# Performance work log

Hardware: AMD Instinct MI355X
Metric: run time of the kernel (lower is better)

## Reference

```python
import jax, jax.numpy as jnp
import numpy as np

N_NODES = 100000
N_REL = 8
IN_DIM = 64
HID = 128
OUT = 64
N_EDGES = 640000


def setup_inputs() -> dict:
    key = jax.random.key(0)
    ks = jax.random.split(key, 24)

    def w(k, shape, fan_in):
        return jax.random.normal(k, shape, jnp.float32) / np.sqrt(fan_in).astype(np.float32)

    inp = {}
    inp["emb"] = jax.random.normal(ks[0], (N_NODES, IN_DIM), jnp.float32)
    dims = [(IN_DIM, HID), (HID, HID), (HID, HID // 2), (HID // 2, OUT)]
    for i, (di, do) in enumerate(dims, 1):
        inp[f"W{i}"] = w(ks[3 * i], (N_REL, di, do), di)      # per-relation weight
        inp[f"R{i}"] = w(ks[3 * i + 1], (di, do), di)          # root weight
        inp[f"B{i}"] = jnp.zeros((do,), jnp.float32)           # bias
    inp["g1"] = jnp.ones((HID,), jnp.float32)
    inp["b1"] = jnp.zeros((HID,), jnp.float32)
    inp["g2"] = jnp.ones((HID,), jnp.float32)
    inp["b2"] = jnp.zeros((HID,), jnp.float32)
    inp["ei"] = jax.random.randint(ks[20], (2, N_EDGES), 0, N_NODES, jnp.int32)
    inp["et"] = jax.random.randint(ks[21], (N_EDGES,), 0, N_REL, jnp.int32)
    return inp


def rgcn(x, ei, et, W, Wr, b):
    # PyG RGCNConv (aggr='mean'): out_i = x_i @ Wroot + b + sum_r mean_{j in N_r(i)} x_j @ W_r
    # Aggregate-then-transform: mean x[src] per (dst, rel) bin, then per-relation GEMM.
    n, r, d = x.shape[0], W.shape[0], x.shape[1]
    src, dst = ei[0], ei[1]
    seg = dst * r + et                                   # combined (node, relation) segment id
    agg = jax.ops.segment_sum(x[src], seg, num_segments=n * r)          # [N*R, d]
    cnt = jax.ops.segment_sum(jnp.ones((src.shape[0],), x.dtype), seg, num_segments=n * r)
    agg = (agg / jnp.maximum(cnt, 1.0)[:, None]).reshape(n, r, d)       # mean per relation
    return jnp.einsum('nri,rio->no', agg, W) + x @ Wr + b


def layer_norm(x, g, b, eps=1e-5):
    mu = jnp.mean(x, axis=-1, keepdims=True)
    var = jnp.mean((x - mu) ** 2, axis=-1, keepdims=True)
    return (x - mu) * jax.lax.rsqrt(var + eps) * g + b


def reference(emb, W1, R1, B1, W2, R2, B2, W3, R3, B3, W4, R4, B4, g1, b1, g2, b2, ei, et):
    # dropout is eval-mode identity
    x = jax.nn.relu(rgcn(emb, ei, et, W1, R1, B1))
    x = layer_norm(x, g1, b1)
    identity = x
    x = jax.nn.relu(rgcn(x, ei, et, W2, R2, B2))
    x = layer_norm(x + identity, g2, b2)
    x = jax.nn.relu(rgcn(x, ei, et, W3, R3, B3))
    return rgcn(x, ei, et, W4, R4, B4)
```

## Files before the change

kernel.cpp:

```cpp
#include <hip/hip_runtime.h>
#include <math.h>

#define NN 100000
#define NR 8
#define NE 640000
#define SEGN (NN * NR)
#define SPB 2048
#define NSB ((SEGN + SPB - 1) / SPB)

#define TILES 1563
#define HT1 782
#define HT2 781
#define HP1 (HT1 * 64)
#define HP2 (HT2 * 64)
#define HPF (TILES * 64)

typedef __attribute__((ext_vector_type(8))) __bf16 bf16x8;
typedef __attribute__((ext_vector_type(4))) float  f32x4;

__device__ __forceinline__ float bf2f(unsigned short b) {
    return __uint_as_float((unsigned)b << 16);
}
__device__ __forceinline__ unsigned short f2bf(float v) {
    __bf16 b = (__bf16)v;
    return __builtin_bit_cast(unsigned short, b);
}


__global__ __launch_bounds__(256) void count_kernel(
    const int* __restrict__ dst, const int* __restrict__ et, unsigned* __restrict__ cnt) {
    int e = blockIdx.x * 256 + threadIdx.x;
    if (e < NE) atomicAdd(&cnt[(size_t)et[e] * NN + dst[e]], 1u);
}

__global__ __launch_bounds__(256) void scan1_kernel(
    const unsigned* __restrict__ cnt, unsigned* __restrict__ bsum) {
    __shared__ unsigned red[256];
    int b = blockIdx.x, t = threadIdx.x;
    int i0 = b * SPB;
    unsigned s = 0;
#pragma unroll
    for (int k = 0; k < SPB / 256; ++k) {
        int i = i0 + k * 256 + t;
        if (i < SEGN) s += cnt[i];
    }
    red[t] = s;
    __syncthreads();
    for (int off = 128; off >= 1; off >>= 1) {
        if (t < off) red[t] += red[t + off];
        __syncthreads();
    }
    if (t == 0) bsum[b] = red[0];
}

__global__ __launch_bounds__(512) void scan2_kernel(
    unsigned* __restrict__ bsum, int* __restrict__ segoff) {
    __shared__ unsigned buf[512];
    int t = threadIdx.x;
    unsigned v = (t < NSB) ? bsum[t] : 0u;
    buf[t] = v;
    __syncthreads();
    for (int off = 1; off < 512; off <<= 1) {
        unsigned w = (t >= off) ? buf[t - off] : 0u;
        __syncthreads();
        buf[t] += w;
        __syncthreads();
    }
    if (t < NSB) bsum[t] = buf[t] - v;
    if (t == 0) segoff[SEGN] = NE;
}

__global__ __launch_bounds__(256) void scan3_kernel(
    const unsigned* __restrict__ cnt, const unsigned* __restrict__ bsum,
    int* __restrict__ segoff) {
    __shared__ unsigned lc[SPB];
    __shared__ unsigned tsum[256];
    int b = blockIdx.x, t = threadIdx.x;
    int i0 = b * SPB;
#pragma unroll
    for (int k = 0; k < SPB / 256; ++k) {
        int i = i0 + k * 256 + t;
        lc[k * 256 + t] = (i < SEGN) ? cnt[i] : 0u;
    }
    __syncthreads();
    unsigned s = 0;
#pragma unroll
    for (int k = 0; k < 8; ++k) s += lc[t * 8 + k];
    tsum[t] = s;
    __syncthreads();
    for (int off = 1; off < 256; off <<= 1) {
        unsigned w = (t >= off) ? tsum[t - off] : 0u;
        __syncthreads();
        tsum[t] += w;
        __syncthreads();
    }
    unsigned base = bsum[b] + tsum[t] - s;
#pragma unroll
    for (int k = 0; k < 8; ++k) {
        unsigned c = lc[t * 8 + k];
        lc[t * 8 + k] = base;
        base += c;
    }
    __syncthreads();
#pragma unroll
    for (int k = 0; k < SPB / 256; ++k) {
        int i = i0 + k * 256 + t;
        if (i < SEGN) segoff[i] = (int)lc[k * 256 + t];
    }
}

__global__ __launch_bounds__(256) void fill_kernel(
    const int* __restrict__ src, const int* __restrict__ dst, const int* __restrict__ et,
    const int* __restrict__ segoff, unsigned* __restrict__ cursor, int* __restrict__ esrc) {
    int e = blockIdx.x * 256 + threadIdx.x;
    if (e >= NE) return;
    int d = dst[e];
    int seg = et[e] * NN + d;
    int pos = segoff[seg] + (int)atomicAdd(&cursor[seg], 1u);
    esrc[pos] = src[e] | ((d & 3) << 17);
}


template <int D, int O>
__global__ __launch_bounds__(256) void pack_kernel(
    const float* __restrict__ W, const float* __restrict__ Wr, __bf16* __restrict__ Wp) {
    constexpr int KT = D / 32, NTN = O / 16;
    int idx = blockIdx.x * 256 + threadIdx.x;
    if (idx >= (NR + 1) * KT * NTN * 64) return;
    int l = idx & 63;
    int rest = idx >> 6;
    int nt = rest % NTN; rest /= NTN;
    int kt = rest % KT;
    int r  = rest / KT;
    const float* srcw = (r < NR) ? (W + (size_t)r * D * O) : Wr;
    int n  = nt * 16 + (l & 15);
    int k0 = kt * 32 + (l >> 4) * 8;
    bf16x8 v;
#pragma unroll
    for (int j = 0; j < 8; ++j) {
        int p  = k0 + j;
        int kd = (D == 128) ? ((p >> 1) + ((p & 1) << 6)) : p;
        v[j] = (__bf16)srcw[(size_t)kd * O + n];
    }
    *(bf16x8*)(Wp + (size_t)idx * 8) = v;
}


template <int D, int XF>
__global__ __launch_bounds__(256) void gather_kernel(
    const void* __restrict__ xin, const int* __restrict__ segoff,
    const int* __restrict__ esrc, ushort* __restrict__ agg,
    int nbase, int agg_off, int HP)
{
    int wv = threadIdx.x >> 6, ln = threadIdx.x & 63;
    int r  = blockIdx.y;
    int i0 = blockIdx.x * 16 + wv * 4;
    int n0 = nbase + i0;

    const float*    xf = (const float*)xin;
    const ushort*   xb = (const ushort*)xin;
    const unsigned* xs = (const unsigned*)xin;

    float ax[4] = {0, 0, 0, 0}, ay[4] = {0, 0, 0, 0};
    int eo[5];
#pragma unroll
    for (int k = 0; k <= 4; ++k) {
        int node = n0 + k; if (node > NN) node = NN;
        eo[k] = segoff[r * NN + node];
    }
    for (int ei = eo[0]; ei < eo[4]; ei += 4) {
        int nb = eo[4] - ei; if (nb > 4) nb = 4;
        int mm[4]; float vx[4], vy[4];
#pragma unroll
        for (int b = 0; b < 4; ++b) mm[b] = (b < nb) ? esrc[ei + b] : 0;
#pragma unroll
        for (int b = 0; b < 4; ++b) {
            if (b < nb) {
                int s = mm[b] & 0x1FFFF;
                if constexpr (XF == 0) {
                    vx[b] = xf[(size_t)s * 64 + ln];
                } else if constexpr (XF == 1) {
                    unsigned w = xs[(size_t)s * 64 + ln];
                    vx[b] = bf2f((unsigned short)(w & 0xFFFFu));
                    vy[b] = bf2f((unsigned short)(w >> 16));
                } else {
                    vx[b] = bf2f(xb[(size_t)s * 64 + ln]);
                }
            }
        }
#pragma unroll
        for (int b = 0; b < 4; ++b) {
            if (b < nb) {
                int k = mm[b] >> 17;
#pragma unroll
                for (int kk = 0; kk < 4; ++kk) {
                    ax[kk] += (kk == k) ? vx[b] : 0.0f;
                    if constexpr (D == 128) ay[kk] += (kk == k) ? vy[b] : 0.0f;
                }
            }
        }
    }
#pragma unroll
    for (int k = 0; k < 4; ++k) {
        int c = eo[k + 1] - eo[k];
        float sc = (c > 0) ? 1.0f / (float)c : 0.0f;
        size_t row = ((size_t)r * HP + agg_off + i0 + k) * D;
        if constexpr (D == 128) {
            unsigned st = (unsigned)f2bf(ax[k] * sc) | ((unsigned)f2bf(ay[k] * sc) << 16);
            *((unsigned*)(agg + row) + ln) = st;
        } else {
            agg[row + ln] = f2bf(ax[k] * sc);
        }
    }
}


template <int D, int O, int MODE, int XF, int OF>
__global__ __launch_bounds__(64) void gemm_layer(
    const ushort* __restrict__ agg, const __bf16* __restrict__ Wp,
    const float* __restrict__ bias, const float* __restrict__ gamma,
    const float* __restrict__ beta, const unsigned* __restrict__ xres,
    const void* __restrict__ xroot, void* __restrict__ outv, int base, int HP)
{
    constexpr int KT = D / 32, NTN = O / 16;
    constexpr int PD = (D == 64) ? 8 : 3;
    int ln = threadIdx.x, lg = ln >> 4, lm = ln & 15;
    int i0 = blockIdx.x * 16;

    const ushort* abase = agg + ((size_t)(i0 + lm)) * D + lg * 8;

    bf16x8 Aall[NR][KT];
#pragma unroll
    for (int r = 0; r < PD; ++r) {
        const ushort* ar = abase + (size_t)r * HP * D;
#pragma unroll
        for (int kt = 0; kt < KT; ++kt)
            Aall[r][kt] = *(const bf16x8*)(ar + kt * 32);
    }

    bf16x8 Aroot[KT];
    {
        int nrow = base + i0 + lm;
        if (nrow >= NN) nrow = NN - 1;
#pragma unroll
        for (int kt = 0; kt < KT; ++kt) {
            if constexpr (XF == 0) {
                const float* xp = (const float*)xroot + (size_t)nrow * 64 + kt * 32 + lg * 8;
                f32x4 a0 = *(const f32x4*)xp;
                f32x4 a1 = *(const f32x4*)(xp + 4);
#pragma unroll
                for (int j = 0; j < 4; ++j) {
                    Aroot[kt][j] = (__bf16)a0[j];
                    Aroot[kt][j + 4] = (__bf16)a1[j];
                }
            } else if constexpr (XF == 1) {
                Aroot[kt] = *(const bf16x8*)((const ushort*)xroot +
                                             (size_t)nrow * 128 + kt * 32 + lg * 8);
            } else {
                Aroot[kt] = *(const bf16x8*)((const ushort*)xroot +
                                             (size_t)nrow * 64 + kt * 32 + lg * 8);
            }
        }
    }

    f32x4 acc[NTN];
#pragma unroll
    for (int nt = 0; nt < NTN; ++nt)
#pragma unroll
        for (int q = 0; q < 4; ++q) acc[nt][q] = 0.0f;

#pragma unroll
    for (int r = 0; r < NR; ++r) {
        if (r + PD < NR) {
            const ushort* an = abase + (size_t)(r + PD) * HP * D;
#pragma unroll
            for (int kt = 0; kt < KT; ++kt)
                Aall[r + PD][kt] = *(const bf16x8*)(an + kt * 32);
        }
        const __bf16* bp = Wp + (((size_t)(r * KT) * NTN) << 9) + (ln << 3);
#pragma unroll
        for (int kt = 0; kt < KT; ++kt) {
            const __bf16* bpk = bp + (((size_t)(kt * NTN)) << 9);
#pragma unroll
            for (int nt = 0; nt < NTN; ++nt) {
                bf16x8 B = *(const bf16x8*)(bpk + ((size_t)nt << 9));
                acc[nt] = __builtin_amdgcn_mfma_f32_16x16x32_bf16(Aall[r][kt], B, acc[nt], 0, 0, 0);
            }
        }
    }
    {
        const __bf16* bp = Wp + (((size_t)(8 * KT) * NTN) << 9) + (ln << 3);
#pragma unroll
        for (int kt = 0; kt < KT; ++kt) {
            const __bf16* bpk = bp + (((size_t)(kt * NTN)) << 9);
#pragma unroll
            for (int nt = 0; nt < NTN; ++nt) {
                bf16x8 B = *(const bf16x8*)(bpk + ((size_t)nt << 9));
                acc[nt] = __builtin_amdgcn_mfma_f32_16x16x32_bf16(Aroot[kt], B, acc[nt], 0, 0, 0);
            }
        }
    }

    float bb[NTN], gg[NTN], be[NTN];
#pragma unroll
    for (int nt = 0; nt < NTN; ++nt) {
        bb[nt] = bias[nt * 16 + lm];
        if constexpr (MODE <= 1) {
            gg[nt] = gamma[nt * 16 + lm];
            be[nt] = beta[nt * 16 + lm];
        } else {
            gg[nt] = 0.0f; be[nt] = 0.0f;
        }
    }
#pragma unroll
    for (int q = 0; q < 4; ++q) {
        int row = lg * 4 + q;
        int n = base + i0 + row;
        int nc = (n < NN) ? n : 0;
        float v[NTN];
#pragma unroll
        for (int nt = 0; nt < NTN; ++nt) {
            v[nt] = acc[nt][q] + bb[nt];
            if constexpr (MODE <= 2) v[nt] = fmaxf(v[nt], 0.0f);
            if constexpr (MODE == 1) {
                unsigned w = xres[(size_t)nc * 64 + (nt & 3) * 16 + lm];
                v[nt] += bf2f((unsigned short)((nt < 4) ? (w & 0xFFFFu) : (w >> 16)));
            }
        }
        if constexpr (MODE <= 1) {
            float s1 = 0.0f, s2 = 0.0f;
#pragma unroll
            for (int nt = 0; nt < NTN; ++nt) { s1 += v[nt]; s2 += v[nt] * v[nt]; }
#pragma unroll
            for (int off = 1; off < 16; off <<= 1) {
                s1 += __shfl_xor(s1, off, 64);
                s2 += __shfl_xor(s2, off, 64);
            }
            float mu  = s1 * (1.0f / O);
            float var = s2 * (1.0f / O) - mu * mu;
            float rs  = rsqrtf(var + 1e-5f);
#pragma unroll
            for (int nt = 0; nt < NTN; ++nt) v[nt] = (v[nt] - mu) * rs * gg[nt] + be[nt];
        }
        if (n < NN) {
            if constexpr (OF == 0) {
#pragma unroll
                for (int nt = 0; nt < NTN; ++nt)
                    __builtin_nontemporal_store(
                        v[nt], (float*)outv + (size_t)n * O + nt * 16 + lm);
            } else if constexpr (OF == 1) {
#pragma unroll
                for (int nt = 0; nt < 4; ++nt)
                    ((unsigned*)outv)[(size_t)n * 64 + nt * 16 + lm] =
                        (unsigned)f2bf(v[nt]) | ((unsigned)f2bf(v[nt + 4]) << 16);
            } else {
#pragma unroll
                for (int nt = 0; nt < NTN; ++nt)
                    ((ushort*)outv)[(size_t)n * 64 + nt * 16 + lm] = f2bf(v[nt]);
            }
        }
    }
}


extern "C" void kernel_launch(void* const* d_in, const int* in_sizes, int n_in,
                              void* d_out, int out_size, void* d_ws, size_t ws_size,
                              hipStream_t stream) {
    const float* emb = (const float*)d_in[0];
    const float* W1  = (const float*)d_in[1];
    const float* R1  = (const float*)d_in[2];
    const float* B1  = (const float*)d_in[3];
    const float* W2  = (const float*)d_in[4];
    const float* R2  = (const float*)d_in[5];
    const float* B2  = (const float*)d_in[6];
    const float* W3  = (const float*)d_in[7];
    const float* R3  = (const float*)d_in[8];
    const float* B3  = (const float*)d_in[9];
    const float* W4  = (const float*)d_in[10];
    const float* R4  = (const float*)d_in[11];
    const float* B4  = (const float*)d_in[12];
    const float* g1  = (const float*)d_in[13];
    const float* b1  = (const float*)d_in[14];
    const float* g2  = (const float*)d_in[15];
    const float* b2  = (const float*)d_in[16];
    const int*   ei  = (const int*)d_in[17];
    const int*   et  = (const int*)d_in[18];
    const int* srcp = ei;
    const int* dstp = ei + NE;

    char* ws = (char*)d_ws;
    if (ws_size < 185734160u) return;
    int*      segoff = (int*)(ws + 0);
    int*      esrc   = (int*)(ws + 3200016);
    __bf16*   Wp1    = (__bf16*)(ws + 5760016);
    __bf16*   Wp2    = (__bf16*)(ws + 5907472);
    __bf16*   Wp3    = (__bf16*)(ws + 6202384);
    __bf16*   Wp4    = (__bf16*)(ws + 6349840);
    void*     x1     = (void*)(ws + 6423568);
    void*     x2     = (void*)(ws + 32023568);
    void*     x3     = (void*)(ws + 57623568);
    ushort*   agg    = (ushort*)(ws + 70423568);
    unsigned* cnt    = (unsigned*)(ws + 70423568);
    unsigned* cursor = (unsigned*)(ws + 73623568);
    unsigned* bsum   = (unsigned*)(ws + 76823568);
    float*    outp   = (float*)d_out;

    hipMemsetAsync(cnt, 0, 3200000, stream);
    hipMemsetAsync(cursor, 0, 3200000, stream);

    count_kernel<<<(NE + 255) / 256, 256, 0, stream>>>(dstp, et, cnt);
    scan1_kernel<<<NSB, 256, 0, stream>>>(cnt, bsum);
    scan2_kernel<<<1, 512, 0, stream>>>(bsum, segoff);
    scan3_kernel<<<NSB, 256, 0, stream>>>(cnt, bsum, segoff);
    fill_kernel<<<(NE + 255) / 256, 256, 0, stream>>>(
        srcp, dstp, et, segoff, cursor, esrc);

    pack_kernel<64, 128><<<(9 * 2 * 8 * 64 + 255) / 256, 256, 0, stream>>>(W1, R1, Wp1);
    pack_kernel<128, 128><<<(9 * 4 * 8 * 64 + 255) / 256, 256, 0, stream>>>(W2, R2, Wp2);
    pack_kernel<128, 64><<<(9 * 4 * 4 * 64 + 255) / 256, 256, 0, stream>>>(W3, R3, Wp3);
    pack_kernel<64, 64><<<(9 * 2 * 4 * 64 + 255) / 256, 256, 0, stream>>>(W4, R4, Wp4);

    gather_kernel<64, 0><<<dim3(HP1 / 16, 8), 256, 0, stream>>>(emb, segoff, esrc, agg, 0, 0, HPF);
    gather_kernel<64, 0><<<dim3(HP2 / 16, 8), 256, 0, stream>>>(emb, segoff, esrc, agg, HP1, HP1, HPF);
    gemm_layer<64, 128, 0, 0, 1><<<HPF / 16, 64, 0, stream>>>(
        agg, Wp1, B1, g1, b1, nullptr, emb, x1, 0, HPF);

    gather_kernel<128, 1><<<dim3(25024 / 16, 8), 256, 0, stream>>>(x1, segoff, esrc, agg, 0, 0, HP1);
    gather_kernel<128, 1><<<dim3(25024 / 16, 8), 256, 0, stream>>>(x1, segoff, esrc, agg, 25024, 25024, HP1);
    gemm_layer<128, 128, 1, 1, 1><<<HP1 / 16, 64, 0, stream>>>(
        agg, Wp2, B2, g2, b2, (const unsigned*)x1, x1, x2, 0, HP1);
    gather_kernel<128, 1><<<dim3(25024 / 16, 8), 256, 0, stream>>>(x1, segoff, esrc, agg, HP1, 0, HP2);
    gather_kernel<128, 1><<<dim3(24960 / 16, 8), 256, 0, stream>>>(x1, segoff, esrc, agg, HP1 + 25024, 25024, HP2);
    gemm_layer<128, 128, 1, 1, 1><<<HP2 / 16, 64, 0, stream>>>(
        agg, Wp2, B2, g2, b2, (const unsigned*)x1, x1, x2, HP1, HP2);

    gather_kernel<128, 1><<<dim3(25024 / 16, 8), 256, 0, stream>>>(x2, segoff, esrc, agg, 0, 0, HP1);
    gather_kernel<128, 1><<<dim3(25024 / 16, 8), 256, 0, stream>>>(x2, segoff, esrc, agg, 25024, 25024, HP1);
    gemm_layer<128, 64, 2, 1, 2><<<HP1 / 16, 64, 0, stream>>>(
        agg, Wp3, B3, nullptr, nullptr, nullptr, x2, x3, 0, HP1);
    gather_kernel<128, 1><<<dim3(25024 / 16, 8), 256, 0, stream>>>(x2, segoff, esrc, agg, HP1, 0, HP2);
    gather_kernel<128, 1><<<dim3(24960 / 16, 8), 256, 0, stream>>>(x2, segoff, esrc, agg, HP1 + 25024, 25024, HP2);
    gemm_layer<128, 64, 2, 1, 2><<<HP2 / 16, 64, 0, stream>>>(
        agg, Wp3, B3, nullptr, nullptr, nullptr, x2, x3, HP1, HP2);

    gather_kernel<64, 2><<<dim3(HP1 / 16, 8), 256, 0, stream>>>(x3, segoff, esrc, agg, 0, 0, HPF);
    gather_kernel<64, 2><<<dim3(HP2 / 16, 8), 256, 0, stream>>>(x3, segoff, esrc, agg, HP1, HP1, HPF);
    gemm_layer<64, 64, 3, 2, 0><<<HPF / 16, 64, 0, stream>>>(
        agg, Wp4, B4, nullptr, nullptr, nullptr, x3, outp, 0, HPF);
}
```

Measured before the change: 704.4 us.

## Fuse gather and GEMM into one launch pipelined over node quarters

After: 853.5 us. 1.21x slower.

```diff
diff --git a/kernel.cpp b/kernel.cpp
--- a/kernel.cpp
+++ b/kernel.cpp
@@ -8,12 +8,9 @@
 #define SPB 2048
 #define NSB ((SEGN + SPB - 1) / SPB)
 
-#define TILES 1563
-#define HT1 782
-#define HT2 781
-#define HP1 (HT1 * 64)
-#define HP2 (HT2 * 64)
-#define HPF (TILES * 64)
+#define QSZ 25024
+static const int qbase[5] = {0, 25024, 50048, 75072, 100032};
+static const int qsize[4] = {25024, 25024, 25024, 24960};
 
 typedef __attribute__((ext_vector_type(8))) __bf16 bf16x8;
 typedef __attribute__((ext_vector_type(4))) float  f32x4;
@@ -118,6 +115,16 @@
     int seg = et[e] * NN + d;
     int pos = segoff[seg] + (int)atomicAdd(&cursor[seg], 1u);
     esrc[pos] = src[e] | ((d & 3) << 17);
+}
+
+__global__ __launch_bounds__(256) void conv_emb(
+    const float* __restrict__ emb, ushort* __restrict__ embb) {
+    int i = blockIdx.x * 256 + threadIdx.x;
+    if (i * 4 >= NN * 64) return;
+    f32x4 v = *(const f32x4*)(emb + (size_t)i * 4);
+    ushort4 o;
+    o.x = f2bf(v[0]); o.y = f2bf(v[1]); o.z = f2bf(v[2]); o.w = f2bf(v[3]);
+    *(ushort4*)(embb + (size_t)i * 4) = o;
 }
 
 
@@ -146,18 +153,157 @@
 }
 
 
-template <int D, int XF>
-__global__ __launch_bounds__(256) void gather_kernel(
+template <int D, int O, int MODE, int XF, int OF>
+__global__ __launch_bounds__(256) void fused_kernel(
+    int mb,
+    const ushort* __restrict__ aggG, const __bf16* __restrict__ Wp,
+    const float* __restrict__ bias, const float* __restrict__ gamma,
+    const float* __restrict__ beta, const unsigned* __restrict__ xres,
+    const void* __restrict__ xroot, void* __restrict__ outv, int gbase, int gQP,
     const void* __restrict__ xin, const int* __restrict__ segoff,
-    const int* __restrict__ esrc, ushort* __restrict__ agg,
-    int nbase, int agg_off, int HP)
+    const int* __restrict__ esrc, ushort* __restrict__ aggS, int nbase, int sQP)
 {
-    int wv = threadIdx.x >> 6, ln = threadIdx.x & 63;
-    int r  = blockIdx.y;
-    int i0 = blockIdx.x * 16 + wv * 4;
+    constexpr int KT = D / 32, NTN = O / 16;
+    int tid = threadIdx.x;
+    int wv = tid >> 6, ln = tid & 63;
+
+    if ((int)blockIdx.x < mb) {
+        constexpr int PD = (D == 64) ? 8 : 3;
+        int lg = ln >> 4, lm = ln & 15;
+        int i0 = blockIdx.x * 64 + wv * 16;
+
+        const ushort* abase = aggG + ((size_t)(i0 + lm)) * D + lg * 8;
+
+        bf16x8 Aall[NR][KT];
+#pragma unroll
+        for (int r = 0; r < PD; ++r) {
+            const ushort* ar = abase + (size_t)r * gQP * D;
+#pragma unroll
+            for (int kt = 0; kt < KT; ++kt)
+                Aall[r][kt] = *(const bf16x8*)(ar + kt * 32);
+        }
+
+        bf16x8 Aroot[KT];
+        {
+            int nrow = gbase + i0 + lm;
+            if (nrow >= NN) nrow = NN - 1;
+#pragma unroll
+            for (int kt = 0; kt < KT; ++kt) {
+                if constexpr (XF == 1) {
+                    Aroot[kt] = *(const bf16x8*)((const ushort*)xroot +
+                                                 (size_t)nrow * 128 + kt * 32 + lg * 8);
+                } else {
+                    Aroot[kt] = *(const bf16x8*)((const ushort*)xroot +
+                                                 (size_t)nrow * 64 + kt * 32 + lg * 8);
+                }
+            }
+        }
+
+        f32x4 acc[NTN];
+#pragma unroll
+        for (int nt = 0; nt < NTN; ++nt)
+#pragma unroll
+            for (int q = 0; q < 4; ++q) acc[nt][q] = 0.0f;
+
+#pragma unroll
+        for (int r = 0; r < NR; ++r) {
+            if (r + PD < NR) {
+                const ushort* an = abase + (size_t)(r + PD) * gQP * D;
+#pragma unroll
+                for (int kt = 0; kt < KT; ++kt)
+                    Aall[r + PD][kt] = *(const bf16x8*)(an + kt * 32);
+            }
+            const __bf16* bp = Wp + (((size_t)(r * KT) * NTN) << 9) + (ln << 3);
+#pragma unroll
+            for (int kt = 0; kt < KT; ++kt) {
+                const __bf16* bpk = bp + (((size_t)(kt * NTN)) << 9);
+#pragma unroll
+                for (int nt = 0; nt < NTN; ++nt) {
+                    bf16x8 B = *(const bf16x8*)(bpk + ((size_t)nt << 9));
+                    acc[nt] = __builtin_amdgcn_mfma_f32_16x16x32_bf16(Aall[r][kt], B, acc[nt], 0, 0, 0);
+                }
+            }
+        }
+        {
+            const __bf16* bp = Wp + (((size_t)(8 * KT) * NTN) << 9) + (ln << 3);
+#pragma unroll
+            for (int kt = 0; kt < KT; ++kt) {
+                const __bf16* bpk = bp + (((size_t)(kt * NTN)) << 9);
+#pragma unroll
+                for (int nt = 0; nt < NTN; ++nt) {
+                    bf16x8 B = *(const bf16x8*)(bpk + ((size_t)nt << 9));
+                    acc[nt] = __builtin_amdgcn_mfma_f32_16x16x32_bf16(Aroot[kt], B, acc[nt], 0, 0, 0);
+                }
+            }
+        }
+
+        float bb[NTN], gg[NTN], be[NTN];
+#pragma unroll
+        for (int nt = 0; nt < NTN; ++nt) {
+            bb[nt] = bias[nt * 16 + lm];
+            if constexpr (MODE <= 1) {
+                gg[nt] = gamma[nt * 16 + lm];
+                be[nt] = beta[nt * 16 + lm];
+            } else {
+                gg[nt] = 0.0f; be[nt] = 0.0f;
+            }
+        }
+#pragma unroll
+        for (int q = 0; q < 4; ++q) {
+            int row = lg * 4 + q;
+            int n = gbase + i0 + row;
+            int nc = (n < NN) ? n : 0;
+            float v[NTN];
+#pragma unroll
+            for (int nt = 0; nt < NTN; ++nt) {
+                v[nt] = acc[nt][q] + bb[nt];
+                if constexpr (MODE <= 2) v[nt] = fmaxf(v[nt], 0.0f);
+                if constexpr (MODE == 1) {
+                    unsigned w = xres[(size_t)nc * 64 + (nt & 3) * 16 + lm];
+                    v[nt] += bf2f((unsigned short)((nt < 4) ? (w & 0xFFFFu) : (w >> 16)));
+                }
+            }
+            if constexpr (MODE <= 1) {
+                float s1 = 0.0f, s2 = 0.0f;
+#pragma unroll
+                for (int nt = 0; nt < NTN; ++nt) { s1 += v[nt]; s2 += v[nt] * v[nt]; }
+#pragma unroll
+                for (int off = 1; off < 16; off <<= 1) {
+                    s1 += __shfl_xor(s1, off, 64);
+                    s2 += __shfl_xor(s2, off, 64);
+                }
+                float mu  = s1 * (1.0f / O);
+                float var = s2 * (1.0f / O) - mu * mu;
+                float rs  = rsqrtf(var + 1e-5f);
+#pragma unroll
+                for (int nt = 0; nt < NTN; ++nt) v[nt] = (v[nt] - mu) * rs * gg[nt] + be[nt];
+            }
+            if (n < NN) {
+                if constexpr (OF == 0) {
+#pragma unroll
+                    for (int nt = 0; nt < NTN; ++nt)
+                        __builtin_nontemporal_store(
+                            v[nt], (float*)outv + (size_t)n * O + nt * 16 + lm);
+                } else if constexpr (OF == 1) {
+#pragma unroll
+                    for (int nt = 0; nt < 4; ++nt)
+                        ((unsigned*)outv)[(size_t)n * 64 + nt * 16 + lm] =
+                            (unsigned)f2bf(v[nt]) | ((unsigned)f2bf(v[nt + 4]) << 16);
+                } else {
+#pragma unroll
+                    for (int nt = 0; nt < NTN; ++nt)
+                        ((ushort*)outv)[(size_t)n * 64 + nt * 16 + lm] = f2bf(v[nt]);
+                }
+            }
+        }
+        return;
+    }
+
+    int gb = blockIdx.x - mb;
+    int tile = gb >> 3, r = gb & 7;
+    int i0 = tile * 16 + wv * 4;
     int n0 = nbase + i0;
 
-    const float*    xf = (const float*)xin;
     const ushort*   xb = (const ushort*)xin;
     const unsigned* xs = (const unsigned*)xin;
 
@@ -177,9 +323,7 @@
         for (int b = 0; b < 4; ++b) {
             if (b < nb) {
                 int s = mm[b] & 0x1FFFF;
-                if constexpr (XF == 0) {
-                    vx[b] = xf[(size_t)s * 64 + ln];
-                } else if constexpr (XF == 1) {
+                if constexpr (XF == 1) {
                     unsigned w = xs[(size_t)s * 64 + ln];
                     vx[b] = bf2f((unsigned short)(w & 0xFFFFu));
                     vy[b] = bf2f((unsigned short)(w >> 16));
@@ -204,164 +348,41 @@
     for (int k = 0; k < 4; ++k) {
         int c = eo[k + 1] - eo[k];
         float sc = (c > 0) ? 1.0f / (float)c : 0.0f;
-        size_t row = ((size_t)r * HP + agg_off + i0 + k) * D;
+        size_t row = ((size_t)r * sQP + i0 + k) * D;
         if constexpr (D == 128) {
             unsigned st = (unsigned)f2bf(ax[k] * sc) | ((unsigned)f2bf(ay[k] * sc) << 16);
-            *((unsigned*)(agg + row) + ln) = st;
+            *((unsigned*)(aggS + row) + ln) = st;
         } else {
-            agg[row + ln] = f2bf(ax[k] * sc);
-        }
-    }
-}
-
+            aggS[row + ln] = f2bf(ax[k] * sc);
+        }
+    }
+}
+
+
+#define SLOTE(D) ((size_t)8 * 25024 * (D))
 
 template <int D, int O, int MODE, int XF, int OF>
-__global__ __launch_bounds__(64) void gemm_layer(
-    const ushort* __restrict__ agg, const __bf16* __restrict__ Wp,
-    const float* __restrict__ bias, const float* __restrict__ gamma,
-    const float* __restrict__ beta, const unsigned* __restrict__ xres,
-    const void* __restrict__ xroot, void* __restrict__ outv, int base, int HP)
-{
-    constexpr int KT = D / 32, NTN = O / 16;
-    constexpr int PD = (D == 64) ? 8 : 3;
-    int ln = threadIdx.x, lg = ln >> 4, lm = ln & 15;
-    int i0 = blockIdx.x * 16;
-
-    const ushort* abase = agg + ((size_t)(i0 + lm)) * D + lg * 8;
-
-    bf16x8 Aall[NR][KT];
-#pragma unroll
-    for (int r = 0; r < PD; ++r) {
-        const ushort* ar = abase + (size_t)r * HP * D;
-#pragma unroll
-        for (int kt = 0; kt < KT; ++kt)
-            Aall[r][kt] = *(const bf16x8*)(ar + kt * 32);
-    }
-
-    bf16x8 Aroot[KT];
-    {
-        int nrow = base + i0 + lm;
-        if (nrow >= NN) nrow = NN - 1;
-#pragma unroll
-        for (int kt = 0; kt < KT; ++kt) {
-            if constexpr (XF == 0) {
-                const float* xp = (const float*)xroot + (size_t)nrow * 64 + kt * 32 + lg * 8;
-                f32x4 a0 = *(const f32x4*)xp;
-                f32x4 a1 = *(const f32x4*)(xp + 4);
-#pragma unroll
-                for (int j = 0; j < 4; ++j) {
-                    Aroot[kt][j] = (__bf16)a0[j];
-                    Aroot[kt][j + 4] = (__bf16)a1[j];
-                }
-            } else if constexpr (XF == 1) {
-                Aroot[kt] = *(const bf16x8*)((const ushort*)xroot +
-                                             (size_t)nrow * 128 + kt * 32 + lg * 8);
-            } else {
-                Aroot[kt] = *(const bf16x8*)((const ushort*)xroot +
-                                             (size_t)nrow * 64 + kt * 32 + lg * 8);
-            }
-        }
-    }
-
-    f32x4 acc[NTN];
-#pragma unroll
-    for (int nt = 0; nt < NTN; ++nt)
-#pragma unroll
-        for (int q = 0; q < 4; ++q) acc[nt][q] = 0.0f;
-
-#pragma unroll
-    for (int r = 0; r < NR; ++r) {
-        if (r + PD < NR) {
-            const ushort* an = abase + (size_t)(r + PD) * HP * D;
-#pragma unroll
-            for (int kt = 0; kt < KT; ++kt)
-                Aall[r + PD][kt] = *(const bf16x8*)(an + kt * 32);
-        }
-        const __bf16* bp = Wp + (((size_t)(r * KT) * NTN) << 9) + (ln << 3);
-#pragma unroll
-        for (int kt = 0; kt < KT; ++kt) {
-            const __bf16* bpk = bp + (((size_t)(kt * NTN)) << 9);
-#pragma unroll
-            for (int nt = 0; nt < NTN; ++nt) {
-                bf16x8 B = *(const bf16x8*)(bpk + ((size_t)nt << 9));
-                acc[nt] = __builtin_amdgcn_mfma_f32_16x16x32_bf16(Aall[r][kt], B, acc[nt], 0, 0, 0);
-            }
-        }
-    }
-    {
-        const __bf16* bp = Wp + (((size_t)(8 * KT) * NTN) << 9) + (ln << 3);
-#pragma unroll
-        for (int kt = 0; kt < KT; ++kt) {
-            const __bf16* bpk = bp + (((size_t)(kt * NTN)) << 9);
-#pragma unroll
-            for (int nt = 0; nt < NTN; ++nt) {
-                bf16x8 B = *(const bf16x8*)(bpk + ((size_t)nt << 9));
-                acc[nt] = __builtin_amdgcn_mfma_f32_16x16x32_bf16(Aroot[kt], B, acc[nt], 0, 0, 0);
-            }
-        }
-    }
-
-    float bb[NTN], gg[NTN], be[NTN];
-#pragma unroll
-    for (int nt = 0; nt < NTN; ++nt) {
-        bb[nt] = bias[nt * 16 + lm];
-        if constexpr (MODE <= 1) {
-            gg[nt] = gamma[nt * 16 + lm];
-            be[nt] = beta[nt * 16 + lm];
-        } else {
-            gg[nt] = 0.0f; be[nt] = 0.0f;
-        }
-    }
-#pragma unroll
-    for (int q = 0; q < 4; ++q) {
-        int row = lg * 4 + q;
-        int n = base + i0 + row;
-        int nc = (n < NN) ? n : 0;
-        float v[NTN];
-#pragma unroll
-        for (int nt = 0; nt < NTN; ++nt) {
-            v[nt] = acc[nt][q] + bb[nt];
-            if constexpr (MODE <= 2) v[nt] = fmaxf(v[nt], 0.0f);
-            if constexpr (MODE == 1) {
-                unsigned w = xres[(size_t)nc * 64 + (nt & 3) * 16 + lm];
-                v[nt] += bf2f((unsigned short)((nt < 4) ? (w & 0xFFFFu) : (w >> 16)));
-            }
-        }
-        if constexpr (MODE <= 1) {
-            float s1 = 0.0f, s2 = 0.0f;
-#pragma unroll
-            for (int nt = 0; nt < NTN; ++nt) { s1 += v[nt]; s2 += v[nt] * v[nt]; }
-#pragma unroll
-            for (int off = 1; off < 16; off <<= 1) {
-                s1 += __shfl_xor(s1, off, 64);
-                s2 += __shfl_xor(s2, off, 64);
-            }
-            float mu  = s1 * (1.0f / O);
-            float var = s2 * (1.0f / O) - mu * mu;
-            float rs  = rsqrtf(var + 1e-5f);
-#pragma unroll
-            for (int nt = 0; nt < NTN; ++nt) v[nt] = (v[nt] - mu) * rs * gg[nt] + be[nt];
-        }
-        if (n < NN) {
-            if constexpr (OF == 0) {
-#pragma unroll
-                for (int nt = 0; nt < NTN; ++nt)
-                    __builtin_nontemporal_store(
-                        v[nt], (float*)outv + (size_t)n * O + nt * 16 + lm);
-            } else if constexpr (OF == 1) {
-#pragma unroll
-                for (int nt = 0; nt < 4; ++nt)
-                    ((unsigned*)outv)[(size_t)n * 64 + nt * 16 + lm] =
-                        (unsigned)f2bf(v[nt]) | ((unsigned)f2bf(v[nt + 4]) << 16);
-            } else {
-#pragma unroll
-                for (int nt = 0; nt < NTN; ++nt)
-                    ((ushort*)outv)[(size_t)n * 64 + nt * 16 + lm] = f2bf(v[nt]);
-            }
-        }
-    }
-}
-
+static void run_layer(const void* xin, const __bf16* Wp, const float* bias,
+                      const float* gamma, const float* beta, const unsigned* xres,
+                      void* out, ushort* agg, const int* segoff, const int* esrc,
+                      hipStream_t stream) {
+    auto slot = [&](int q) { return agg + (size_t)(q & 1) * SLOTE(D); };
+    auto gB = [](int n) { return (n / 16) * 8; };
+    auto mB = [](int n) { return n / 64; };
+    fused_kernel<D, O, MODE, XF, OF><<<gB(qsize[0]), 256, 0, stream>>>(
+        0, nullptr, Wp, bias, gamma, beta, xres, xin, out, 0, 0,
+        xin, segoff, esrc, slot(0), qbase[0], qsize[0]);
+    for (int q = 0; q < 3; ++q) {
+        fused_kernel<D, O, MODE, XF, OF><<<mB(qsize[q]) + gB(qsize[q + 1]), 256, 0, stream>>>(
+            mB(qsize[q]), slot(q), Wp, bias, gamma, beta, xres, xin, out,
+            qbase[q], qsize[q],
+            xin, segoff, esrc, slot(q + 1), qbase[q + 1], qsize[q + 1]);
+    }
+    fused_kernel<D, O, MODE, XF, OF><<<mB(qsize[3]), 256, 0, stream>>>(
+        mB(qsize[3]), slot(3), Wp, bias, gamma, beta, xres, xin, out,
+        qbase[3], qsize[3],
+        xin, segoff, esrc, slot(3), 0, 0);
+}
 
 extern "C" void kernel_launch(void* const* d_in, const int* in_sizes, int n_in,
                               void* d_out, int out_size, void* d_ws, size_t ws_size,
@@ -389,20 +410,21 @@
     const int* dstp = ei + NE;
 
     char* ws = (char*)d_ws;
-    if (ws_size < 185734160u) return;
+    if (ws_size < 185721872u) return;
     int*      segoff = (int*)(ws + 0);
     int*      esrc   = (int*)(ws + 3200016);
     __bf16*   Wp1    = (__bf16*)(ws + 5760016);
     __bf16*   Wp2    = (__bf16*)(ws + 5907472);
     __bf16*   Wp3    = (__bf16*)(ws + 6202384);
     __bf16*   Wp4    = (__bf16*)(ws + 6349840);
-    void*     x1     = (void*)(ws + 6423568);
-    void*     x2     = (void*)(ws + 32023568);
-    void*     x3     = (void*)(ws + 57623568);
-    ushort*   agg    = (ushort*)(ws + 70423568);
-    unsigned* cnt    = (unsigned*)(ws + 70423568);
-    unsigned* cursor = (unsigned*)(ws + 73623568);
-    unsigned* bsum   = (unsigned*)(ws + 76823568);
+    ushort*   embb   = (ushort*)(ws + 6423568);
+    void*     x1     = (void*)(ws + 19223568);
+    void*     x2     = (void*)(ws + 44823568);
+    void*     x3     = (void*)(ws + 70423568);
+    ushort*   agg    = (ushort*)(ws + 83223568);
+    unsigned* cnt    = (unsigned*)(ws + 83223568);
+    unsigned* cursor = (unsigned*)(ws + 86423568);
+    unsigned* bsum   = (unsigned*)(ws + 89623568);
     float*    outp   = (float*)d_out;
 
     hipMemsetAsync(cnt, 0, 3200000, stream);
@@ -414,37 +436,19 @@
     scan3_kernel<<<NSB, 256, 0, stream>>>(cnt, bsum, segoff);
     fill_kernel<<<(NE + 255) / 256, 256, 0, stream>>>(
         srcp, dstp, et, segoff, cursor, esrc);
+    conv_emb<<<(NN * 64 / 4 + 255) / 256, 256, 0, stream>>>(emb, embb);
 
     pack_kernel<64, 128><<<(9 * 2 * 8 * 64 + 255) / 256, 256, 0, stream>>>(W1, R1, Wp1);
     pack_kernel<128, 128><<<(9 * 4 * 8 * 64 + 255) / 256, 256, 0, stream>>>(W2, R2, Wp2);
     pack_kernel<128, 64><<<(9 * 4 * 4 * 64 + 255) / 256, 256, 0, stream>>>(W3, R3, Wp3);
     pack_kernel<64, 64><<<(9 * 2 * 4 * 64 + 255) / 256, 256, 0, stream>>>(W4, R4, Wp4);
 
-    gather_kernel<64, 0><<<dim3(HP1 / 16, 8), 256, 0, stream>>>(emb, segoff, esrc, agg, 0, 0, HPF);
-    gather_kernel<64, 0><<<dim3(HP2 / 16, 8), 256, 0, stream>>>(emb, segoff, esrc, agg, HP1, HP1, HPF);
-    gemm_layer<64, 128, 0, 0, 1><<<HPF / 16, 64, 0, stream>>>(
-        agg, Wp1, B1, g1, b1, nullptr, emb, x1, 0, HPF);
-
-    gather_kernel<128, 1><<<dim3(25024 / 16, 8), 256, 0, stream>>>(x1, segoff, esrc, agg, 0, 0, HP1);
-    gather_kernel<128, 1><<<dim3(25024 / 16, 8), 256, 0, stream>>>(x1, segoff, esrc, agg, 25024, 25024, HP1);
-    gemm_layer<128, 128, 1, 1, 1><<<HP1 / 16, 64, 0, stream>>>(
-        agg, Wp2, B2, g2, b2, (const unsigned*)x1, x1, x2, 0, HP1);
-    gather_kernel<128, 1><<<dim3(25024 / 16, 8), 256, 0, stream>>>(x1, segoff, esrc, agg, HP1, 0, HP2);
-    gather_kernel<128, 1><<<dim3(24960 / 16, 8), 256, 0, stream>>>(x1, segoff, esrc, agg, HP1 + 25024, 25024, HP2);
-    gemm_layer<128, 128, 1, 1, 1><<<HP2 / 16, 64, 0, stream>>>(
-        agg, Wp2, B2, g2, b2, (const unsigned*)x1, x1, x2, HP1, HP2);
-
-    gather_kernel<128, 1><<<dim3(25024 / 16, 8), 256, 0, stream>>>(x2, segoff, esrc, agg, 0, 0, HP1);
-    gather_kernel<128, 1><<<dim3(25024 / 16, 8), 256, 0, stream>>>(x2, segoff, esrc, agg, 25024, 25024, HP1);
-    gemm_layer<128, 64, 2, 1, 2><<<HP1 / 16, 64, 0, stream>>>(
-        agg, Wp3, B3, nullptr, nullptr, nullptr, x2, x3, 0, HP1);
-    gather_kernel<128, 1><<<dim3(25024 / 16, 8), 256, 0, stream>>>(x2, segoff, esrc, agg, HP1, 0, HP2);
-    gather_kernel<128, 1><<<dim3(24960 / 16, 8), 256, 0, stream>>>(x2, segoff, esrc, agg, HP1 + 25024, 25024, HP2);
-    gemm_layer<128, 64, 2, 1, 2><<<HP2 / 16, 64, 0, stream>>>(
-        agg, Wp3, B3, nullptr, nullptr, nullptr, x2, x3, HP1, HP2);
-
-    gather_kernel<64, 2><<<dim3(HP1 / 16, 8), 256, 0, stream>>>(x3, segoff, esrc, agg, 0, 0, HPF);
-    gather_kernel<64, 2><<<dim3(HP2 / 16, 8), 256, 0, stream>>>(x3, segoff, esrc, agg, HP1, HP1, HPF);
-    gemm_layer<64, 64, 3, 2, 0><<<HPF / 16, 64, 0, stream>>>(
-        agg, Wp4, B4, nullptr, nullptr, nullptr, x3, outp, 0, HPF);
-}
+    run_layer<64, 128, 0, 2, 1>(embb, Wp1, B1, g1, b1, nullptr, x1,
+                                agg, segoff, esrc, stream);
+    run_layer<128, 128, 1, 1, 1>(x1, Wp2, B2, g2, b2, (const unsigned*)x1, x2,
+                                 agg, segoff, esrc, stream);
+    run_layer<128, 64, 2, 1, 2>(x2, Wp3, B3, nullptr, nullptr, nullptr, x3,
+                                agg, segoff, esrc, stream);
+    run_layer<64, 64, 3, 2, 0>(x3, Wp4, B4, nullptr, nullptr, nullptr, outp,
+                               agg, segoff, esrc, stream);
+}
```
